# Kernel optimization log

Hardware: AMD Instinct MI355X
Metric: run time of the kernel (lower is better)

## Reference

```python
import jax, jax.numpy as jnp
import numpy as np

CH = 256
CQK = CH // 8
B, H, W = 4, 64, 64


def setup_inputs() -> dict:
    key = jax.random.key(0)
    ks = jax.random.split(key, 8)
    s_qk = 1.0 / np.sqrt(CH)  # MSR init for 1x1 conv: std = 1/sqrt(fan_in)
    x = jax.random.normal(ks[0], (B, CH, H, W), dtype=jnp.float32)
    Wq = jax.random.normal(ks[1], (CQK, CH), dtype=jnp.float32) * s_qk
    bq = jnp.zeros((CQK,), dtype=jnp.float32)
    Wk = jax.random.normal(ks[2], (CQK, CH), dtype=jnp.float32) * s_qk
    bk = jnp.zeros((CQK,), dtype=jnp.float32)
    Wv = jax.random.normal(ks[3], (CH, CH), dtype=jnp.float32) * s_qk
    bv = jnp.zeros((CH,), dtype=jnp.float32)
    # NOTE: module inits gamma=0; use a nonzero value so the attention branch is active
    gamma = jnp.float32(0.5) * jnp.ones((1,), dtype=jnp.float32)
    return {"x": x, "Wq": Wq, "bq": bq, "Wk": Wk, "bk": bk, "Wv": Wv, "bv": bv, "gamma": gamma}


def reference(x, Wq, bq, Wk, bk, Wv, bv, gamma):
    b, c, h, w = x.shape
    n = h * w
    xf = x.reshape(b, c, n)  # [B, C, N]
    # 1x1 convs are per-pixel channel projections
    q = jnp.einsum('oc,bcn->bon', Wq, xf) + bq[:, None]  # [B, C/8, N]
    k = jnp.einsum('oc,bcn->bon', Wk, xf) + bk[:, None]  # [B, C/8, N]
    v = jnp.einsum('oc,bcn->bon', Wv, xf) + bv[:, None]  # [B, C, N]
    # scores[b, i, j] = q[:, i] . k[:, j]  (no scaling, as in source)
    att = jax.nn.softmax(jnp.einsum('bci,bcj->bij', q, k), axis=-1)  # [B, N, N]
    out = jnp.einsum('bcj,bij->bci', v, att).reshape(b, c, h, w)
    return x + gamma[0] * out
```

## Files before the change

### kernel.cpp

```cpp
#include <hip/hip_runtime.h>
#include <hip/hip_bf16.h>

typedef unsigned short u16;
typedef __attribute__((ext_vector_type(8))) __bf16 bf16x8;
typedef __attribute__((ext_vector_type(8))) short s16x8;
typedef __attribute__((ext_vector_type(4))) float f32x4;
typedef __attribute__((ext_vector_type(16))) float f32x16;

#define MFMA16(a, b, c) __builtin_amdgcn_mfma_f32_16x16x32_bf16((a), (b), (c), 0, 0, 0)
#define MFMA32(a, b, c) __builtin_amdgcn_mfma_f32_32x32x16_bf16((a), (b), (c), 0, 0, 0)

#define BN 4
#define CH 256
#define CQK 32
#define NPIX 4096

__device__ __forceinline__ u16 f2bf(float f) {
    __hip_bfloat16 h = __float2bfloat16(f);
    return *reinterpret_cast<u16*>(&h);
}

__device__ __forceinline__ f32x16 zero16() {
    f32x16 z;
#pragma unroll
    for (int i = 0; i < 16; ++i) z[i] = 0.f;
    return z;
}

__device__ __forceinline__ int perm16(int k) {
    return (k & 3) | ((k & 4) << 1) | ((k & 8) >> 1);
}

__global__ void k_transpose(const float* __restrict__ x, u16* __restrict__ xt) {
    __shared__ float xs[64][65];
    int n0 = blockIdx.x * 64, c0 = blockIdx.y * 64, b = blockIdx.z;
    int t = threadIdx.x;
    const float* xp = x + ((size_t)(b * CH + c0)) * NPIX + n0;
#pragma unroll
    for (int it = 0; it < 16; ++it) {
        int idx = it * 256 + t;
        int cc = idx >> 6, nn = idx & 63;
        xs[cc][nn] = xp[(size_t)cc * NPIX + nn];
    }
    __syncthreads();
    u16* op = xt + ((size_t)(b * NPIX + n0)) * CH + c0;
#pragma unroll
    for (int it = 0; it < 16; ++it) {
        int idx = it * 256 + t;
        int nn = idx >> 6, cc = idx & 63;
        op[(size_t)nn * CH + cc] = f2bf(xs[cc][nn]);
    }
}

__global__ void k_wcvt(const float* __restrict__ Wq, const float* __restrict__ Wk,
                       const float* __restrict__ Wv, u16* __restrict__ Wbf) {
    int idx = blockIdx.x * 256 + threadIdx.x;
    int o = idx >> 8, c = idx & 255;
    float v;
    if (o < 32) v = Wq[o * 256 + c];
    else if (o < 64) v = Wk[(o - 32) * 256 + c];
    else v = Wv[(o - 64) * 256 + c];
    Wbf[idx] = f2bf(v);
}

__launch_bounds__(256, 1)
__global__ void k_proj(const u16* __restrict__ Wbf, const u16* __restrict__ xt,
                       const float* __restrict__ bq, const float* __restrict__ bk,
                       const float* __restrict__ bv,
                       u16* __restrict__ qb, u16* __restrict__ kb, u16* __restrict__ vb) {
    int b = blockIdx.y, n0 = blockIdx.x * 64;
    int t = threadIdx.x, w = t >> 6, l = t & 63;
    int lr = l & 15, lg = l >> 4;

    f32x4 acc[5][4];
#pragma unroll
    for (int s = 0; s < 5; ++s)
#pragma unroll
        for (int u = 0; u < 4; ++u) acc[s][u] = f32x4{0.f, 0.f, 0.f, 0.f};

    const u16* xtb = xt + ((size_t)(b * NPIX + n0)) * CH;

#pragma unroll
    for (int kk = 0; kk < 8; ++kk) {
        int kof = kk * 32 + lg * 8;
        bf16x8 af[5], bfr[4];
#pragma unroll
        for (int s = 0; s < 5; ++s) {
            int o = w * 16 + s * 64 + lr;
            af[s] = *reinterpret_cast<const bf16x8*>(Wbf + (size_t)o * 256 + kof);
        }
#pragma unroll
        for (int u = 0; u < 4; ++u) {
            int n = u * 16 + lr;
            bfr[u] = *reinterpret_cast<const bf16x8*>(xtb + (size_t)n * CH + kof);
        }
#pragma unroll
        for (int s = 0; s < 5; ++s)
#pragma unroll
            for (int u = 0; u < 4; ++u) acc[s][u] = MFMA16(af[s], bfr[u], acc[s][u]);
    }

    int lrp = perm16(lr);
#pragma unroll
    for (int s = 0; s < 5; ++s) {
        int o0 = w * 16 + s * 64;
#pragma unroll
        for (int r = 0; r < 4; ++r) {
            int o = o0 + lg * 4 + r;
            float bias = (o < 32) ? bq[o] : (o < 64) ? bk[o - 32] : bv[o - 64];
#pragma unroll
            for (int u = 0; u < 4; ++u) {
                float val = acc[s][u][r] + bias;
                u16 h = f2bf(val);
                if (o < 32) qb[((size_t)b * NPIX + n0 + u * 16 + lr) * CQK + o] = h;
                else if (o < 64) kb[((size_t)b * NPIX + n0 + u * 16 + lr) * CQK + (o - 32)] = h;
                else vb[((size_t)(b * CH + (o - 64))) * NPIX + n0 + u * 16 + lrp] = h;
            }
        }
    }
}

template <int NCHUNK>
__launch_bounds__(256, 2)
__global__ void k_attn2(const u16* __restrict__ qb, const u16* __restrict__ kb,
                        const u16* __restrict__ vb, const float* __restrict__ x,
                        const float* __restrict__ gamma,
                        float* __restrict__ pacc, float* __restrict__ plsum,
                        float* __restrict__ out) {
    constexpr int JCH = NPIX / NCHUNK;
    constexpr int NT = JCH / 32;
    int it = blockIdx.x, s = blockIdx.y, b = blockIdx.z;
    int t = threadIdx.x, w = t >> 6, l = t & 63;
    int lr = l & 31, hi = l >> 5;
    int i0 = it * 128;
    int j0 = s * JCH;

    __shared__ u16 vlds[2][256][40];
    __shared__ float lsl[128];

    const u16* qrow = qb + ((size_t)b * NPIX + i0 + w * 32 + lr) * CQK;
    bf16x8 qf0 = *(const bf16x8*)(qrow + hi * 8);
    bf16x8 qf1 = *(const bf16x8*)(qrow + 16 + hi * 8);

    const u16* kbase = kb + (size_t)b * NPIX * CQK;
    const u16* vbase = vb + (size_t)(b * CH) * NPIX;

    f32x16 acc[8];
#pragma unroll
    for (int ct = 0; ct < 8; ++ct) acc[ct] = zero16();
    float lsum_p = 0.f;

    int srow = t >> 2, swg = t & 3;
    bf16x8 vst[4];
    bf16x8 kc0, kc1;

    auto vload = [&](int jt) {
#pragma unroll
        for (int m = 0; m < 4; ++m)
            vst[m] = *(const bf16x8*)(vbase + (size_t)(64 * m + srow) * NPIX +
                                      j0 + jt * 32 + swg * 8);
    };
    auto vwrite = [&](int buf) {
#pragma unroll
        for (int m = 0; m < 4; ++m)
            *(bf16x8*)(&vlds[buf][64 * m + srow][swg * 8]) = vst[m];
    };
    auto kload = [&](int jt) {
        const u16* kr = kbase + (size_t)(j0 + jt * 32 + lr) * CQK;
        kc0 = *(const bf16x8*)(kr + hi * 8);
        kc1 = *(const bf16x8*)(kr + 16 + hi * 8);
    };
    auto qk_soft = [&](bf16x8& pa0, bf16x8& pa1) {
        f32x16 sf = MFMA32(kc0, qf0, zero16());
        sf = MFMA32(kc1, qf1, sf);
        s16x8 w0, w1;
#pragma unroll
        for (int e = 0; e < 8; ++e) {
            float p0 = __expf(sf[e] - 32.0f);
            float p1 = __expf(sf[8 + e] - 32.0f);
            lsum_p += p0 + p1;
            w0[e] = (short)f2bf(p0);
            w1[e] = (short)f2bf(p1);
        }
        pa0 = __builtin_bit_cast(bf16x8, w0);
        pa1 = __builtin_bit_cast(bf16x8, w1);
    };
    auto pv = [&](int buf, bf16x8 pa0, bf16x8 pa1) {
        __builtin_amdgcn_s_setprio(1);
#pragma unroll
        for (int ct = 0; ct < 8; ++ct) {
            const u16* vr = &vlds[buf][ct * 32 + lr][hi * 8];
            bf16x8 vf0 = *(const bf16x8*)(vr);
            bf16x8 vf1 = *(const bf16x8*)(vr + 16);
            acc[ct] = MFMA32(pa0, vf0, acc[ct]);
            acc[ct] = MFMA32(pa1, vf1, acc[ct]);
        }
        __builtin_amdgcn_s_setprio(0);
    };

    bf16x8 paA0, paA1, paB0, paB1;
    vload(0);
    vwrite(0);
    kload(0);
    vload(1);
    __syncthreads();
    qk_soft(paA0, paA1);
    kload(1);

    for (int tp = 0; tp < NT; tp += 2) {
        bool m2 = (tp + 2 < NT);
        bool m3 = (tp + 3 < NT);
        __syncthreads();
        vwrite(1);
        if (m2) vload(tp + 2);
        qk_soft(paB0, paB1);
        if (m2) kload(tp + 2);
        pv(0, paA0, paA1);
        __syncthreads();
        if (m2) vwrite(0);
        if (m3) vload(tp + 3);
        if (m2) qk_soft(paA0, paA1);
        if (m3) kload(tp + 3);
        pv(1, paB0, paB1);
    }

    lsum_p += __shfl_xor(lsum_p, 32);

    if constexpr (NCHUNK == 1) {
        float g = gamma[0];
        if (l < 32) lsl[w * 32 + l] = g / lsum_p;
        __syncthreads();
#pragma unroll
        for (int ct = 0; ct < 8; ++ct) {
            int c = ct * 32 + lr;
            const float* xp = x + ((size_t)(b * CH + c)) * NPIX + i0;
            float* op = out + ((size_t)(b * CH + c)) * NPIX + i0;
#pragma unroll
            for (int r = 0; r < 16; ++r) {
                int il = w * 32 + (r & 3) + 8 * (r >> 2) + 4 * hi;
                op[il] = xp[il] + acc[ct][r] * lsl[il];
            }
        }
    } else {
        size_t pbase = ((((size_t)s * BN + b) * 32 + it) * 256) * 128;
#pragma unroll
        for (int ct = 0; ct < 8; ++ct) {
            int c = ct * 32 + lr;
#pragma unroll
            for (int q = 0; q < 4; ++q) {
                int il0 = w * 32 + 8 * q + 4 * hi;
                f32x4 vv = {acc[ct][4 * q], acc[ct][4 * q + 1],
                            acc[ct][4 * q + 2], acc[ct][4 * q + 3]};
                *(f32x4*)(pacc + pbase + (size_t)c * 128 + il0) = vv;
            }
        }
        if (l < 32)
            plsum[(((size_t)s * BN + b) * 32 + it) * 128 + w * 32 + l] = lsum_p;
    }
}

template <int NCHUNK>
__global__ void k_reduce(const float* __restrict__ pacc, const float* __restrict__ plsum,
                         const float* __restrict__ x, const float* __restrict__ gamma,
                         float* __restrict__ out) {
    int cg = blockIdx.x, it = blockIdx.y, b = blockIdx.z;
    int t = threadIdx.x;
    int c0 = cg * 32;
    __shared__ float invl[128];

    if (t < 128) {
        float lt = 0.f;
#pragma unroll
        for (int s = 0; s < NCHUNK; ++s)
            lt += plsum[(((size_t)s * BN + b) * 32 + it) * 128 + t];
        invl[t] = gamma[0] / lt;
    }
    __syncthreads();

    const size_t chunk_stride = (size_t)BN * 32 * 256 * 128;
    size_t base = (((size_t)b * 32 + it) * 256 + c0) * 128;

#pragma unroll
    for (int k = 0; k < 4; ++k) {
        int v = k * 256 + t;
        int cl = v >> 5;
        int iv = (v & 31) * 4;
        size_t off = base + (size_t)cl * 128 + iv;
        f32x4 a = {0.f, 0.f, 0.f, 0.f};
#pragma unroll
        for (int s = 0; s < NCHUNK; ++s) {
            f32x4 p = *(const f32x4*)(pacc + (size_t)s * chunk_stride + off);
            a += p;
        }
        f32x4 il4 = *(const f32x4*)(&invl[iv]);
        size_t oi = ((size_t)(b * CH + c0 + cl)) * NPIX + it * 128 + iv;
        f32x4 xi = *(const f32x4*)(x + oi);
        f32x4 r = xi + a * il4;
        *(f32x4*)(out + oi) = r;
    }
}

extern "C" void kernel_launch(void* const* d_in, const int* in_sizes, int n_in,
                              void* d_out, int out_size, void* d_ws, size_t ws_size,
                              hipStream_t stream) {
    const float* x = (const float*)d_in[0];
    const float* Wq = (const float*)d_in[1];
    const float* bq = (const float*)d_in[2];
    const float* Wk = (const float*)d_in[3];
    const float* bk = (const float*)d_in[4];
    const float* Wv = (const float*)d_in[5];
    const float* bv = (const float*)d_in[6];
    const float* gamma = (const float*)d_in[7];
    float* out = (float*)d_out;

    char* ws = (char*)d_ws;
    u16* xt = (u16*)(ws);
    u16* Wbf = (u16*)(ws + 8388608);
    u16* qb = (u16*)(ws + 8388608 + 163840);
    u16* kb = (u16*)(ws + 8388608 + 163840 + 1048576);
    u16* vb = (u16*)(ws + 8388608 + 163840 + 2097152);
    const size_t base_end = 8388608 + 163840 + 2097152 + 8388608;
    float* pacc = (float*)(ws + base_end);

    hipLaunchKernelGGL(k_transpose, dim3(64, 4, 4), dim3(256), 0, stream, x, xt);
    hipLaunchKernelGGL(k_wcvt, dim3(320), dim3(256), 0, stream, Wq, Wk, Wv, Wbf);
    hipLaunchKernelGGL(k_proj, dim3(64, 4), dim3(256), 0, stream, Wbf, xt, bq, bk, bv, qb, kb, vb);

    const size_t pacc4 = (size_t)4 * BN * NPIX * CH * 4;
    const size_t pls4 = (size_t)4 * BN * NPIX * 4;
    const size_t pacc2 = pacc4 / 2, pls2 = pls4 / 2;

    if (ws_size >= base_end + pacc4 + pls4) {
        float* plsum = (float*)(ws + base_end + pacc4);
        hipLaunchKernelGGL(k_attn2<4>, dim3(32, 4, 4), dim3(256), 0, stream,
                           qb, kb, vb, x, gamma, pacc, plsum, out);
        hipLaunchKernelGGL(k_reduce<4>, dim3(8, 32, 4), dim3(256), 0, stream,
                           pacc, plsum, x, gamma, out);
    } else if (ws_size >= base_end + pacc2 + pls2) {
        float* plsum = (float*)(ws + base_end + pacc2);
        hipLaunchKernelGGL(k_attn2<2>, dim3(32, 2, 4), dim3(256), 0, stream,
                           qb, kb, vb, x, gamma, pacc, plsum, out);
        hipLaunchKernelGGL(k_reduce<2>, dim3(8, 32, 4), dim3(256), 0, stream,
                           pacc, plsum, x, gamma, out);
    } else {
        hipLaunchKernelGGL(k_attn2<1>, dim3(32, 1, 4), dim3(256), 0, stream,
                           qb, kb, vb, x, gamma, pacc, pacc, out);
    }
}
```

Measured before the change: 96.23 us.

## Triple-buffer swizzled V tiles, truncate P to bf16, store partials as bf16

Rewrites the attention main loop with a three-stage LDS ring for V tiles, XOR-swizzled rows in place of padding, and a single barrier per tile. The barrier waits only on LDS counters, so global loads can stay in flight. Probabilities are converted to bf16 by truncation instead of rounding. Split-chunk partial accumulators are stored as bf16, halving partial write and read traffic in the reduce kernel. The cost is lower precision in the partial sums and in P, and the loop-carried P registers add some register pressure.

```diff
diff --git a/kernel.cpp b/kernel.cpp
--- a/kernel.cpp
+++ b/kernel.cpp
@@ -3,9 +3,11 @@
 
 typedef unsigned short u16;
 typedef __attribute__((ext_vector_type(8))) __bf16 bf16x8;
-typedef __attribute__((ext_vector_type(8))) short s16x8;
+typedef __attribute__((ext_vector_type(8))) unsigned short u16x8;
 typedef __attribute__((ext_vector_type(4))) float f32x4;
 typedef __attribute__((ext_vector_type(16))) float f32x16;
+typedef __attribute__((ext_vector_type(4))) unsigned int u32x4;
+typedef __attribute__((ext_vector_type(2))) unsigned int u32x2;
 
 #define MFMA16(a, b, c) __builtin_amdgcn_mfma_f32_16x16x32_bf16((a), (b), (c), 0, 0, 0)
 #define MFMA32(a, b, c) __builtin_amdgcn_mfma_f32_32x32x16_bf16((a), (b), (c), 0, 0, 0)
@@ -18,6 +20,18 @@
 __device__ __forceinline__ u16 f2bf(float f) {
     __hip_bfloat16 h = __float2bfloat16(f);
     return *reinterpret_cast<u16*>(&h);
+}
+
+__device__ __forceinline__ unsigned pack2(float a, float b) {
+    return (unsigned)f2bf(a) | ((unsigned)f2bf(b) << 16);
+}
+
+__device__ __forceinline__ unsigned packtr(float a, float b) {
+    return (__float_as_uint(b) & 0xffff0000u) | (__float_as_uint(a) >> 16);
+}
+
+__device__ __forceinline__ float bf2f(u16 v) {
+    return __uint_as_float(((unsigned)v) << 16);
 }
 
 __device__ __forceinline__ f32x16 zero16() {
@@ -122,10 +136,10 @@
 
 template <int NCHUNK>
 __launch_bounds__(256, 2)
-__global__ void k_attn2(const u16* __restrict__ qb, const u16* __restrict__ kb,
+__global__ void k_attn5(const u16* __restrict__ qb, const u16* __restrict__ kb,
                         const u16* __restrict__ vb, const float* __restrict__ x,
                         const float* __restrict__ gamma,
-                        float* __restrict__ pacc, float* __restrict__ plsum,
+                        u16* __restrict__ pacc, float* __restrict__ plsum,
                         float* __restrict__ out) {
     constexpr int JCH = NPIX / NCHUNK;
     constexpr int NT = JCH / 32;
@@ -135,7 +149,7 @@
     int i0 = it * 128;
     int j0 = s * JCH;
 
-    __shared__ u16 vlds[2][256][40];
+    __shared__ u16 vlds[3][256][32];
     __shared__ float lsl[128];
 
     const u16* qrow = qb + ((size_t)b * NPIX + i0 + w * 32 + lr) * CQK;
@@ -150,78 +164,83 @@
     for (int ct = 0; ct < 8; ++ct) acc[ct] = zero16();
     float lsum_p = 0.f;
 
-    int srow = t >> 2, swg = t & 3;
+    int srow = t >> 2, sslot = t & 3;
+    int wslot = (sslot ^ (srow & 3)) * 8;
     bf16x8 vst[4];
     bf16x8 kc0, kc1;
 
-    auto vload = [&](int jt) {
+    auto vload = [&](int tt) {
 #pragma unroll
         for (int m = 0; m < 4; ++m)
             vst[m] = *(const bf16x8*)(vbase + (size_t)(64 * m + srow) * NPIX +
-                                      j0 + jt * 32 + swg * 8);
+                                      j0 + tt * 32 + sslot * 8);
     };
     auto vwrite = [&](int buf) {
+        u16* base = &vlds[buf][0][0];
 #pragma unroll
         for (int m = 0; m < 4; ++m)
-            *(bf16x8*)(&vlds[buf][64 * m + srow][swg * 8]) = vst[m];
-    };
-    auto kload = [&](int jt) {
-        const u16* kr = kbase + (size_t)(j0 + jt * 32 + lr) * CQK;
+            *(bf16x8*)(base + (64 * m + srow) * 32 + wslot) = vst[m];
+    };
+    auto kload = [&](int tt) {
+        const u16* kr = kbase + (size_t)(j0 + tt * 32 + lr) * CQK;
         kc0 = *(const bf16x8*)(kr + hi * 8);
         kc1 = *(const bf16x8*)(kr + 16 + hi * 8);
     };
-    auto qk_soft = [&](bf16x8& pa0, bf16x8& pa1) {
-        f32x16 sf = MFMA32(kc0, qf0, zero16());
-        sf = MFMA32(kc1, qf1, sf);
-        s16x8 w0, w1;
-#pragma unroll
-        for (int e = 0; e < 8; ++e) {
-            float p0 = __expf(sf[e] - 32.0f);
-            float p1 = __expf(sf[8 + e] - 32.0f);
-            lsum_p += p0 + p1;
-            w0[e] = (short)f2bf(p0);
-            w1[e] = (short)f2bf(p1);
-        }
-        pa0 = __builtin_bit_cast(bf16x8, w0);
-        pa1 = __builtin_bit_cast(bf16x8, w1);
-    };
-    auto pv = [&](int buf, bf16x8 pa0, bf16x8 pa1) {
-        __builtin_amdgcn_s_setprio(1);
+    auto qkexp = [&](bf16x8 k0, bf16x8 k1, bf16x8& p0, bf16x8& p1) {
+        f32x16 sf = MFMA32(k0, qf0, zero16());
+        sf = MFMA32(k1, qf1, sf);
+        float P[16];
+#pragma unroll
+        for (int e = 0; e < 16; ++e) {
+            P[e] = __expf(sf[e] - 32.0f);
+            lsum_p += P[e];
+        }
+        u32x4 a = {packtr(P[0], P[1]), packtr(P[2], P[3]),
+                   packtr(P[4], P[5]), packtr(P[6], P[7])};
+        u32x4 c = {packtr(P[8], P[9]), packtr(P[10], P[11]),
+                   packtr(P[12], P[13]), packtr(P[14], P[15])};
+        p0 = __builtin_bit_cast(bf16x8, a);
+        p1 = __builtin_bit_cast(bf16x8, c);
+    };
+    auto pv = [&](int buf, bf16x8 p0, bf16x8 p1) {
+        const u16* base = &vlds[buf][0][0];
 #pragma unroll
         for (int ct = 0; ct < 8; ++ct) {
-            const u16* vr = &vlds[buf][ct * 32 + lr][hi * 8];
-            bf16x8 vf0 = *(const bf16x8*)(vr);
-            bf16x8 vf1 = *(const bf16x8*)(vr + 16);
-            acc[ct] = MFMA32(pa0, vf0, acc[ct]);
-            acc[ct] = MFMA32(pa1, vf1, acc[ct]);
-        }
-        __builtin_amdgcn_s_setprio(0);
+            int c = ct * 32 + lr;
+            int sw = lr & 3;
+            bf16x8 vf0 = *(const bf16x8*)(base + c * 32 + ((hi ^ sw) * 8));
+            bf16x8 vf1 = *(const bf16x8*)(base + c * 32 + (((2 + hi) ^ sw) * 8));
+            acc[ct] = MFMA32(p0, vf0, acc[ct]);
+            acc[ct] = MFMA32(p1, vf1, acc[ct]);
+        }
+    };
+    auto lds_barrier = [&]() {
+        asm volatile("s_waitcnt lgkmcnt(0)" ::: "memory");
+        __builtin_amdgcn_s_barrier();
     };
 
     bf16x8 paA0, paA1, paB0, paB1;
     vload(0);
+    kload(0);
     vwrite(0);
-    kload(0);
     vload(1);
-    __syncthreads();
-    qk_soft(paA0, paA1);
-    kload(1);
-
-    for (int tp = 0; tp < NT; tp += 2) {
-        bool m2 = (tp + 2 < NT);
-        bool m3 = (tp + 3 < NT);
-        __syncthreads();
-        vwrite(1);
-        if (m2) vload(tp + 2);
-        qk_soft(paB0, paB1);
-        if (m2) kload(tp + 2);
-        pv(0, paA0, paA1);
-        __syncthreads();
-        if (m2) vwrite(0);
-        if (m3) vload(tp + 3);
-        if (m2) qk_soft(paA0, paA1);
-        if (m3) kload(tp + 3);
-        pv(1, paB0, paB1);
+    lds_barrier();
+    qkexp(kc0, kc1, paA0, paA1);
+    if (1 < NT) kload(1);
+    vwrite(1);
+    if (2 < NT) vload(2);
+
+    int bR = 0, bW = 2;
+    for (int tt = 0; tt < NT; ++tt) {
+        if (tt + 1 < NT) qkexp(kc0, kc1, paB0, paB1);
+        if (tt + 2 < NT) kload(tt + 2);
+        pv(bR, paA0, paA1);
+        if (tt + 2 < NT) vwrite(bW);
+        if (tt + 3 < NT) vload(tt + 3);
+        lds_barrier();
+        if (tt + 1 < NT) { paA0 = paB0; paA1 = paB1; }
+        bR = (bR == 2) ? 0 : bR + 1;
+        bW = (bW == 2) ? 0 : bW + 1;
     }
 
     lsum_p += __shfl_xor(lsum_p, 32);
@@ -249,9 +268,9 @@
 #pragma unroll
             for (int q = 0; q < 4; ++q) {
                 int il0 = w * 32 + 8 * q + 4 * hi;
-                f32x4 vv = {acc[ct][4 * q], acc[ct][4 * q + 1],
-                            acc[ct][4 * q + 2], acc[ct][4 * q + 3]};
-                *(f32x4*)(pacc + pbase + (size_t)c * 128 + il0) = vv;
+                u32x2 pr = {pack2(acc[ct][4 * q], acc[ct][4 * q + 1]),
+                            pack2(acc[ct][4 * q + 2], acc[ct][4 * q + 3])};
+                *(u32x2*)(pacc + pbase + (size_t)c * 128 + il0) = pr;
             }
         }
         if (l < 32)
@@ -260,7 +279,7 @@
 }
 
 template <int NCHUNK>
-__global__ void k_reduce(const float* __restrict__ pacc, const float* __restrict__ plsum,
+__global__ void k_reduce(const u16* __restrict__ pacc, const float* __restrict__ plsum,
                          const float* __restrict__ x, const float* __restrict__ gamma,
                          float* __restrict__ out) {
     int cg = blockIdx.x, it = blockIdx.y, b = blockIdx.z;
@@ -281,22 +300,25 @@
     size_t base = (((size_t)b * 32 + it) * 256 + c0) * 128;
 
 #pragma unroll
-    for (int k = 0; k < 4; ++k) {
+    for (int k = 0; k < 2; ++k) {
         int v = k * 256 + t;
-        int cl = v >> 5;
-        int iv = (v & 31) * 4;
-        size_t off = base + (size_t)cl * 128 + iv;
-        f32x4 a = {0.f, 0.f, 0.f, 0.f};
+        int cl = v >> 4;
+        int io = (v & 15) * 8;
+        size_t off = base + (size_t)cl * 128 + io;
+        f32x4 a0 = {0.f, 0.f, 0.f, 0.f}, a1 = a0;
 #pragma unroll
         for (int s = 0; s < NCHUNK; ++s) {
-            f32x4 p = *(const f32x4*)(pacc + (size_t)s * chunk_stride + off);
-            a += p;
-        }
-        f32x4 il4 = *(const f32x4*)(&invl[iv]);
-        size_t oi = ((size_t)(b * CH + c0 + cl)) * NPIX + it * 128 + iv;
-        f32x4 xi = *(const f32x4*)(x + oi);
-        f32x4 r = xi + a * il4;
-        *(f32x4*)(out + oi) = r;
+            u16x8 p = *(const u16x8*)(pacc + (size_t)s * chunk_stride + off);
+            a0[0] += bf2f(p[0]); a0[1] += bf2f(p[1]); a0[2] += bf2f(p[2]); a0[3] += bf2f(p[3]);
+            a1[0] += bf2f(p[4]); a1[1] += bf2f(p[5]); a1[2] += bf2f(p[6]); a1[3] += bf2f(p[7]);
+        }
+        f32x4 i0v = *(const f32x4*)(&invl[io]);
+        f32x4 i1v = *(const f32x4*)(&invl[io + 4]);
+        size_t oi = ((size_t)(b * CH + c0 + cl)) * NPIX + it * 128 + io;
+        f32x4 x0 = *(const f32x4*)(x + oi);
+        f32x4 x1 = *(const f32x4*)(x + oi + 4);
+        *(f32x4*)(out + oi) = x0 + a0 * i0v;
+        *(f32x4*)(out + oi + 4) = x1 + a1 * i1v;
     }
 }
 
@@ -320,30 +342,30 @@
     u16* kb = (u16*)(ws + 8388608 + 163840 + 1048576);
     u16* vb = (u16*)(ws + 8388608 + 163840 + 2097152);
     const size_t base_end = 8388608 + 163840 + 2097152 + 8388608;
-    float* pacc = (float*)(ws + base_end);
+    u16* pacc = (u16*)(ws + base_end);
 
     hipLaunchKernelGGL(k_transpose, dim3(64, 4, 4), dim3(256), 0, stream, x, xt);
     hipLaunchKernelGGL(k_wcvt, dim3(320), dim3(256), 0, stream, Wq, Wk, Wv, Wbf);
     hipLaunchKernelGGL(k_proj, dim3(64, 4), dim3(256), 0, stream, Wbf, xt, bq, bk, bv, qb, kb, vb);
 
-    const size_t pacc4 = (size_t)4 * BN * NPIX * CH * 4;
+    const size_t pacc4 = (size_t)4 * BN * NPIX * CH * 2;
     const size_t pls4 = (size_t)4 * BN * NPIX * 4;
     const size_t pacc2 = pacc4 / 2, pls2 = pls4 / 2;
 
     if (ws_size >= base_end + pacc4 + pls4) {
         float* plsum = (float*)(ws + base_end + pacc4);
-        hipLaunchKernelGGL(k_attn2<4>, dim3(32, 4, 4), dim3(256), 0, stream,
+        hipLaunchKernelGGL(k_attn5<4>, dim3(32, 4, 4), dim3(256), 0, stream,
                            qb, kb, vb, x, gamma, pacc, plsum, out);
         hipLaunchKernelGGL(k_reduce<4>, dim3(8, 32, 4), dim3(256), 0, stream,
                            pacc, plsum, x, gamma, out);
     } else if (ws_size >= base_end + pacc2 + pls2) {
         float* plsum = (float*)(ws + base_end + pacc2);
-        hipLaunchKernelGGL(k_attn2<2>, dim3(32, 2, 4), dim3(256), 0, stream,
+        hipLaunchKernelGGL(k_attn5<2>, dim3(32, 2, 4), dim3(256), 0, stream,
                            qb, kb, vb, x, gamma, pacc, plsum, out);
         hipLaunchKernelGGL(k_reduce<2>, dim3(8, 32, 4), dim3(256), 0, stream,
                            pacc, plsum, x, gamma, out);
     } else {
-        hipLaunchKernelGGL(k_attn2<1>, dim3(32, 1, 4), dim3(256), 0, stream,
-                           qb, kb, vb, x, gamma, pacc, pacc, out);
-    }
-}
+        hipLaunchKernelGGL(k_attn5<1>, dim3(32, 1, 4), dim3(256), 0, stream,
+                           qb, kb, vb, x, gamma, pacc, (float*)pacc, out);
+    }
+}
```

After: 93.25 us. 1.03x faster.
